# Kernel tuning notes

Measured on AMD Instinct MI355X. Metric: run time of the kernel, lower is better.

Reference implementation:

```python
import jax, jax.numpy as jnp
import numpy as np

EPS = 1e-6
DIAG_SIZE = 128  # triu band half-width (init kwarg diag_size)
NEG_INF = -1e9


def feature_map(x):
    # tanh feature map: phi(x) = tanh(x) + 1 (positive feature map)
    return jnp.tanh(x) + 1.0


def causal_dot_product(Q, K, V):
    # Q,K: [N,L,H,E], V: [N,L,H,D]
    # running KV state: S_l = sum_{s<=l} K_s V_s^T, materialized via cumsum
    kv = jnp.cumsum(jnp.einsum('nlhe,nlhd->nlhed', K, V), axis=1)  # [N,L,H,E,D]
    return jnp.einsum('nlhe,nlhed->nlhd', Q, kv)


def setup_inputs() -> dict:
    key = jax.random.key(0)
    k1, k2, k3 = jax.random.split(key, 3)
    N, L, H, E = 2, 2048, 8, 64
    queries = jax.random.normal(k1, (N, L, H, E), dtype=jnp.float32)
    keys = jax.random.normal(k2, (N, L, H, E), dtype=jnp.float32)
    values = jax.random.normal(k3, (N, L, H, E), dtype=jnp.float32)
    key_lengths_mask = jnp.ones((N, L), dtype=jnp.float32)  # all keys valid
    blend = jnp.full((1,), 0.9, dtype=jnp.float32)  # learned blend param (init 0.9)
    return {"queries": queries, "keys": keys, "values": values,
            "key_lengths_mask": key_lengths_mask, "blend": blend}


def reference(queries, keys, values, key_lengths_mask, blend):
    N, L, H, E = queries.shape
    # ---- linear attention path (kernel_1 = tanh, kernel_2 = 'none') ----
    Q1 = feature_map(queries)
    K1 = feature_map(keys) * key_lengths_mask[:, :, None, None]
    Z1 = 1.0 / (jnp.einsum('nlhi,nlhi->nlh', Q1, jnp.cumsum(K1, axis=1)) + EPS)
    LV = causal_dot_product(Q1, K1, values) * Z1[..., None]  # [N,L,H,D]
    # ---- full softmax attention path (banded by triu) ----
    softmax_temp = 1.0 / np.sqrt(E).astype(np.float32)
    QK = jnp.einsum('nlhe,nshe->nhls', queries, keys)  # [N,H,L,L]
    l_idx = jnp.arange(L)[:, None]
    s_idx = jnp.arange(L)[None, :]
    causal_add = jnp.where(s_idx <= l_idx, 0.0, NEG_INF)  # lower-triangular mask
    key_add = jnp.where(key_lengths_mask > 0, 0.0, NEG_INF)  # [N,L]
    logits = softmax_temp * (QK + causal_add[None, None] + key_add[:, None, None, :])
    A = jax.nn.softmax(logits, axis=-1)
    # torch.triu(A, diagonal=-diag_size): keep s >= l - diag_size
    band = s_idx >= (l_idx - DIAG_SIZE)
    A = jnp.where(band[None, None], A, 0.0)
    # dropout: eval mode (identity)
    SV = jnp.einsum('nhls,nshd->nlhd', A, values)
    b = blend[0]
    return b * SV + (1.0 - b) * LV
```

## Files before the change

### kernel.cpp

```cpp
#include <hip/hip_runtime.h>
#include <math.h>

#define N_ 2
#define L_ 2048
#define H_ 8
#define E_ 64
#define D_ 64
#define C_ 128
#define NC (L_/C_)
#define ROWSTRIDE (H_*E_)
#define TEMP 0.125f
#define EPS_F 1e-6f
#define NEG_INF_F (-1e9f)
#define CHUNK_WS (E_*D_ + E_)
#define NCHUNKS (N_*H_*NC)
#define TPAD 136
#define PPAD 72
#define PSTG 136

typedef __attribute__((ext_vector_type(8))) short short8;
typedef __attribute__((ext_vector_type(4))) float f32x4;

__device__ __forceinline__ short f2bf(float x) {
  unsigned u = __float_as_uint(x);
  u += 0x7fffu + ((u >> 16) & 1u);
  return (short)(u >> 16);
}
__device__ __forceinline__ float bf2f(short s) {
  return __uint_as_float(((unsigned)(unsigned short)s) << 16);
}
__device__ __forceinline__ float tanh1f(float x) {
  float e = __expf(-2.f * x);
  return 2.f * __builtin_amdgcn_rcpf(1.f + e);
}

template <typename F>
__device__ __forceinline__ void stage_tile(short* __restrict__ dst,
                                           const float* __restrict__ src, F f) {
  const int t = threadIdx.x;
#pragma unroll
  for (int it = 0; it < 4; ++it) {
    int gi = it * 256 + t;
    int row = gi >> 3, g = gi & 7;
    const float* p = src + row * ROWSTRIDE + g * 8;
    float4 a = *(const float4*)p;
    float4 b = *(const float4*)(p + 4);
    float xs[8] = {a.x, a.y, a.z, a.w, b.x, b.y, b.z, b.w};
    short8 v;
#pragma unroll
    for (int j = 0; j < 8; ++j) v[j] = f2bf(f(xs[j], row));
    *(short8*)(dst + row * 64 + (g ^ (row & 7)) * 8) = v;
  }
}

__device__ __forceinline__ short8 frag_ld(const short* __restrict__ buf,
                                          int rowbase, int hf, int lane) {
  int r = rowbase + (lane & 15);
  int g = (hf * 4 + (lane >> 4)) ^ (r & 7);
  return *(const short8*)(buf + r * 64 + g * 8);
}
__device__ __forceinline__ short8 frag_ldT(const short* __restrict__ buf,
                                           int nbase, int g, int lane) {
  int r = nbase + (lane & 15);
  return *(const short8*)(buf + r * TPAD + g * 8);
}
__device__ __forceinline__ short8 frag_ldP(const short* __restrict__ buf,
                                           int rowbase, int ks, int lane) {
  int r = rowbase + (lane & 15);
  int g = ks * 4 + (lane >> 4);
  return *(const short8*)(buf + r * PPAD + g * 8);
}

extern "C" __global__ void __launch_bounds__(256)
k_pre(const float* __restrict__ Q, const float* __restrict__ K,
      const float* __restrict__ V, const float* __restrict__ mask,
      float* __restrict__ ws, float* __restrict__ part,
      short* __restrict__ pd, short* __restrict__ pp) {
  __shared__ short lds[17408];
  __shared__ float fmsk[C_];
  short* ldsA = lds;
  short* ldsB = lds + 8704;
  const int orig = blockIdx.x;
  const int swz = (orig & 7) * 304 + (orig >> 3);
  const int t = threadIdx.x;
  const int w = t >> 6, lane = t & 63;
  const int col_lo = lane & 15;

  if (swz < 2176) {
    const int nh = swz / 136;
    const int p = swz - nh * 136;
    int qb = (int)((sqrtf(8.f * p + 1.f) - 1.f) * 0.5f);
    while ((qb + 1) * (qb + 2) / 2 <= p) ++qb;
    while (qb * (qb + 1) / 2 > p) --qb;
    const int kb = p - qb * (qb + 1) / 2;
    const int h = nh & (H_ - 1), n = nh >> 3;

    stage_tile(ldsA, Q + ((n * L_ + qb * C_) * H_ + h) * E_,
               [](float x, int) { return x; });
    stage_tile(ldsB, K + ((n * L_ + kb * C_) * H_ + h) * E_,
               [](float x, int) { return x; });
    if (t < C_) fmsk[t] = mask[n * L_ + kb * C_ + t];
    __syncthreads();

    const int rowbase = w * 32;
    short8 afr[2][2];
#pragma unroll
    for (int m = 0; m < 2; ++m)
#pragma unroll
      for (int hh = 0; hh < 2; ++hh)
        afr[m][hh] = frag_ld(ldsA, rowbase + 16 * m, hh, lane);

    f32x4 acc[2][8];
#pragma unroll
    for (int m = 0; m < 2; ++m)
#pragma unroll
      for (int c = 0; c < 8; ++c) acc[m][c] = (f32x4){0.f, 0.f, 0.f, 0.f};

#pragma unroll
    for (int c = 0; c < 8; ++c) {
      short8 b0 = frag_ld(ldsB, 16 * c, 0, lane);
      short8 b1 = frag_ld(ldsB, 16 * c, 1, lane);
#pragma unroll
      for (int m = 0; m < 2; ++m) {
        acc[m][c] = __builtin_amdgcn_mfma_f32_16x16x32_bf16(afr[m][0], b0, acc[m][c], 0, 0, 0);
        acc[m][c] = __builtin_amdgcn_mfma_f32_16x16x32_bf16(afr[m][1], b1, acc[m][c], 0, 0, 0);
      }
    }

    const bool diag = (kb == qb);
    const bool prev = (kb == qb - 1);
    const bool band = diag || prev;
    if (band) __syncthreads();

    float* pout = part + (size_t)(nh * NC + qb) * C_ * 16;
#pragma unroll
    for (int m = 0; m < 2; ++m) {
      const int rbase = rowbase + 16 * m + ((lane >> 4) << 2);
      float rs[4] = {0.f, 0.f, 0.f, 0.f};
#pragma unroll
      for (int c = 0; c < 8; ++c) {
        const int col = 16 * c + col_lo;
        const float madd = (fmsk[col] > 0.f) ? 0.f : NEG_INF_F;
#pragma unroll
        for (int reg = 0; reg < 4; ++reg) {
          float x = acc[m][c][reg] + madd;
          if (diag && col > rbase + reg) x += NEG_INF_F;
          float e = __expf(x * TEMP);
          rs[reg] += e;
          if (band) {
            if (prev && col < rbase + reg) e = 0.f;
            lds[(rbase + reg) * PSTG + col] = f2bf(e);
          }
        }
      }
#pragma unroll
      for (int off = 1; off < 16; off <<= 1) {
#pragma unroll
        for (int reg = 0; reg < 4; ++reg) rs[reg] += __shfl_xor(rs[reg], off);
      }
      if (col_lo == 0) {
#pragma unroll
        for (int reg = 0; reg < 4; ++reg) pout[(rbase + reg) * 16 + kb] = rs[reg];
      }
    }

    if (band) {
      __syncthreads();
      short* pt = (diag ? pd : pp) + (size_t)(nh * NC + qb) * (C_ * C_);
#pragma unroll
      for (int i = 0; i < 8; ++i) {
        int flat = i * 256 + t;
        int row = flat >> 4, g = flat & 15;
        *(short8*)(pt + row * C_ + g * 8) =
            *(const short8*)(lds + row * PSTG + g * 8);
      }
    }
  } else {
    const int id = swz - 2176;
    const int nh = id >> 4, c = id & 15;
    const int h = nh & (H_ - 1), n = nh >> 3;
    const int gbase = ((n * L_ + c * C_) * H_ + h) * E_;
    const int e = t & 63, sb = t >> 6;
    const int mbase = n * L_ + c * C_;
#pragma unroll
    for (int q = 0; q < 4; ++q) {
      int s0 = sb * 32 + q * 8;
      short8 kk, vv;
#pragma unroll
      for (int j = 0; j < 8; ++j) {
        float kx = K[gbase + (s0 + j) * ROWSTRIDE + e];
        kk[j] = f2bf(tanh1f(kx) * mask[mbase + s0 + j]);
        vv[j] = f2bf(V[gbase + (s0 + j) * ROWSTRIDE + e]);
      }
      *(short8*)(ldsA + e * TPAD + (s0 >> 3) * 8) = kk;
      *(short8*)(ldsB + e * TPAD + (s0 >> 3) * 8) = vv;
    }
    __syncthreads();

    f32x4 acc[4];
#pragma unroll
    for (int nn = 0; nn < 4; ++nn) acc[nn] = (f32x4){0.f, 0.f, 0.f, 0.f};
#pragma unroll
    for (int ks = 0; ks < 4; ++ks) {
      short8 a = frag_ldT(ldsB, 16 * w, ks * 4 + (lane >> 4), lane);
#pragma unroll
      for (int nn = 0; nn < 4; ++nn) {
        short8 b = frag_ldT(ldsA, 16 * nn, ks * 4 + (lane >> 4), lane);
        acc[nn] = __builtin_amdgcn_mfma_f32_16x16x32_bf16(a, b, acc[nn], 0, 0, 0);
      }
    }
    float* wsc = ws + (size_t)(nh * NC + c) * CHUNK_WS;
    const int drow = 16 * w + ((lane >> 4) << 2);
#pragma unroll
    for (int nn = 0; nn < 4; ++nn)
#pragma unroll
      for (int reg = 0; reg < 4; ++reg)
        wsc[(16 * nn + col_lo) * D_ + drow + reg] = acc[nn][reg];
    if (t < 64) {
      float s = 0.f;
#pragma unroll
      for (int g = 0; g < 16; ++g) {
        short8 v = *(const short8*)(ldsA + t * TPAD + g * 8);
#pragma unroll
        for (int j = 0; j < 8; ++j) s += bf2f(v[j]);
      }
      wsc[E_ * D_ + t] = s;
    }
  }
}

extern "C" __global__ void __launch_bounds__(256)
k_scan(float* __restrict__ ws) {
  const int bid = blockIdx.x;
  const int swz = (bid & 7) * 34 + (bid >> 3);
  const int nh = swz / 17, seg = swz - nh * 17;
  const int idx = seg * 256 + threadIdx.x;
  if (idx >= CHUNK_WS) return;
  float* base = ws + (size_t)nh * NC * CHUNK_WS + idx;
  float v[NC];
#pragma unroll
  for (int c = 0; c < NC; ++c) v[c] = base[(size_t)c * CHUNK_WS];
  float acc = 0.f;
#pragma unroll
  for (int c = 0; c < NC; ++c) {
    base[(size_t)c * CHUNK_WS] = acc;
    acc += v[c];
  }
}

extern "C" __global__ void __launch_bounds__(256, 2)
k_fused(const float* __restrict__ Q, const float* __restrict__ K,
        const float* __restrict__ V, const float* __restrict__ mask,
        const float* __restrict__ blend, const float* __restrict__ ws,
        const float* __restrict__ part, const short* __restrict__ pd,
        const short* __restrict__ pp, float* __restrict__ out) {
  __shared__ short kbuf[C_ * 64];
  __shared__ short kv[64 * TPAD];
  __shared__ short pbuf[64 * PPAD];
  __shared__ float zlds[64];
  __shared__ float dinv[64];
  __shared__ float ksum[E_];

  const int orig = blockIdx.x;
  const int swz = (orig & 7) * 64 + (orig >> 3);
  const int rh = swz & 1, qb = (swz >> 1) & (NC - 1), nh = swz >> 5;
  const int h = nh & (H_ - 1), n = nh >> 3;
  const int t = threadIdx.x;
  const int w = t >> 6, lane = t & 63;
  const int rowbase = w * 16;
  const int col_lo = lane & 15;
  const int rb = rowbase + ((lane >> 4) << 2);
  const int rtile0 = rh * 64 + rb;
  const int qgbase = ((n * L_ + qb * C_ + rh * 64) * H_ + h) * E_;
  const int kbase_chunk = ((n * L_ + qb * C_) * H_ + h) * E_;
  const float* wsc = ws + (size_t)(nh * NC + qb) * CHUNK_WS;
  const float bl = blend[0];
  const float ob = 1.f - bl;
  const int d = t & 63, sb = t >> 6;
  const bool haveprev = (qb > 0);
  const int kgp = ((n * L_ + (qb - 1) * C_) * H_ + h) * E_;

  {
    const float* mrow = mask + n * L_ + qb * C_;
#pragma unroll
    for (int it = 0; it < 4; ++it) {
      int gi = it * 256 + t, row = gi >> 3, g = gi & 7;
      const float* p = K + kbase_chunk + row * ROWSTRIDE + g * 8;
      float4 a = *(const float4*)p, b = *(const float4*)(p + 4);
      float km = mrow[row];
      float xs[8] = {a.x, a.y, a.z, a.w, b.x, b.y, b.z, b.w};
      short8 v1;
#pragma unroll
      for (int j = 0; j < 8; ++j) v1[j] = f2bf(tanh1f(xs[j]) * km);
      *(short8*)(kbuf + row * 64 + (g ^ (row & 7)) * 8) = v1;
    }
  }
  {
    int eb = t >> 6;
#pragma unroll
    for (int q = 0; q < 2; ++q) {
      int e0 = eb * 16 + q * 8;
      short8 v;
#pragma unroll
      for (int j = 0; j < 8; ++j) v[j] = f2bf(wsc[(e0 + j) * D_ + d]);
      *(short8*)(kv + d * TPAD + (e0 >> 3) * 8) = v;
    }
  }
  if (t < 64) {
    ksum[t] = wsc[E_ * D_ + t];
    const float* pb = part + ((size_t)(nh * NC + qb) * C_ + rh * 64 + t) * 16;
    float4 a = *(const float4*)pb, b = *(const float4*)(pb + 4);
    float4 c = *(const float4*)(pb + 8), d4 = *(const float4*)(pb + 12);
    float vv[16] = {a.x, a.y, a.z, a.w, b.x, b.y, b.z, b.w,
                    c.x, c.y, c.z, c.w, d4.x, d4.y, d4.z, d4.w};
    float s = 0.f;
#pragma unroll
    for (int j = 0; j < 16; ++j) s += (j <= qb) ? vv[j] : 0.f;
    dinv[t] = 1.f / s;
  }
  __syncthreads();

  short8 af1[2];
  {
    const float* qp = Q + qgbase + (rowbase + (lane & 15)) * ROWSTRIDE;
#pragma unroll
    for (int kh = 0; kh < 2; ++kh) {
      int c0 = (kh * 4 + (lane >> 4)) * 8;
      float4 a = *(const float4*)(qp + c0);
      float4 b = *(const float4*)(qp + c0 + 4);
      float xs[8] = {a.x, a.y, a.z, a.w, b.x, b.y, b.z, b.w};
#pragma unroll
      for (int j = 0; j < 8; ++j) af1[kh][j] = f2bf(tanh1f(xs[j]));
    }
  }
  f32x4 c1[8];
#pragma unroll
  for (int ct = 0; ct < 8; ++ct) c1[ct] = (f32x4){0.f, 0.f, 0.f, 0.f};
#pragma unroll
  for (int ct = 0; ct < 8; ++ct) {
    short8 b0 = frag_ld(kbuf, 16 * ct, 0, lane);
    short8 b1 = frag_ld(kbuf, 16 * ct, 1, lane);
    c1[ct] = __builtin_amdgcn_mfma_f32_16x16x32_bf16(af1[0], b0, c1[ct], 0, 0, 0);
    c1[ct] = __builtin_amdgcn_mfma_f32_16x16x32_bf16(af1[1], b1, c1[ct], 0, 0, 0);
  }
  {
    float zz = 0.f;
#pragma unroll
    for (int kh = 0; kh < 2; ++kh) {
      int cb = (kh * 4 + (lane >> 4)) * 8;
#pragma unroll
      for (int j = 0; j < 8; ++j) zz += bf2f(af1[kh][j]) * ksum[cb + j];
    }
    zz += __shfl_xor(zz, 16);
    zz += __shfl_xor(zz, 32);
    if (lane < 16) zlds[rowbase + lane] = zz;
  }
  float rs[4] = {0.f, 0.f, 0.f, 0.f};
#pragma unroll
  for (int ct = 0; ct < 8; ++ct) {
    int col = 16 * ct + col_lo;
#pragma unroll
    for (int reg = 0; reg < 4; ++reg) {
      if (col <= rtile0 + reg) rs[reg] += c1[ct][reg];
      else c1[ct][reg] = 0.f;
    }
  }
#pragma unroll
  for (int off = 1; off < 16; off <<= 1)
#pragma unroll
    for (int reg = 0; reg < 4; ++reg) rs[reg] += __shfl_xor(rs[reg], off);

  f32x4 accO[4];
#pragma unroll
  for (int nn = 0; nn < 4; ++nn) accO[nn] = (f32x4){0.f, 0.f, 0.f, 0.f};
#pragma unroll
  for (int ks = 0; ks < 2; ++ks) {
    short8 bf[4];
#pragma unroll
    for (int nn = 0; nn < 4; ++nn)
      bf[nn] = frag_ldT(kv, 16 * nn, ks * 4 + (lane >> 4), lane);
#pragma unroll
    for (int nn = 0; nn < 4; ++nn)
      accO[nn] = __builtin_amdgcn_mfma_f32_16x16x32_bf16(af1[ks], bf[nn], accO[nn], 0, 0, 0);
  }
  float zrf[4], sdv[4];
#pragma unroll
  for (int reg = 0; reg < 4; ++reg) {
    zrf[reg] = ob / (zlds[rb + reg] + rs[reg] + EPS_F);
    sdv[reg] = bl * dinv[rb + reg];
  }
#pragma unroll
  for (int nn = 0; nn < 4; ++nn)
#pragma unroll
    for (int reg = 0; reg < 4; ++reg) accO[nn][reg] *= zrf[reg];
#pragma unroll
  for (int ct = 0; ct < 8; ++ct)
#pragma unroll
    for (int reg = 0; reg < 4; ++reg) c1[ct][reg] *= zrf[reg];
  __syncthreads();

#pragma unroll
  for (int q = 0; q < 4; ++q) {
    int s0 = sb * 32 + q * 8;
    short8 v;
#pragma unroll
    for (int j = 0; j < 8; ++j) v[j] = f2bf(V[kbase_chunk + (s0 + j) * ROWSTRIDE + d]);
    *(short8*)(kv + d * TPAD + (s0 >> 3) * 8) = v;
  }
  __syncthreads();

#pragma unroll
  for (int hh = 0; hh < 2; ++hh) {
#pragma unroll
    for (int cc = 0; cc < 4; ++cc) {
      int ct = 4 * hh + cc, colh = 16 * cc + col_lo;
#pragma unroll
      for (int reg = 0; reg < 4; ++reg)
        pbuf[(rb + reg) * PPAD + colh] = f2bf(c1[ct][reg]);
    }
#pragma unroll
    for (int ks = 0; ks < 2; ++ks) {
      short8 ap = frag_ldP(pbuf, rowbase, ks, lane);
      short8 bv[4];
#pragma unroll
      for (int nn = 0; nn < 4; ++nn)
        bv[nn] = frag_ldT(kv, 16 * nn, 8 * hh + ks * 4 + (lane >> 4), lane);
#pragma unroll
      for (int nn = 0; nn < 4; ++nn)
        accO[nn] = __builtin_amdgcn_mfma_f32_16x16x32_bf16(ap, bv[nn], accO[nn], 0, 0, 0);
    }
  }

  f32x4 accS[4];
#pragma unroll
  for (int nn = 0; nn < 4; ++nn) accS[nn] = (f32x4){0.f, 0.f, 0.f, 0.f};
  {
    const short* ps = pd + (size_t)(nh * NC + qb) * (C_ * C_) + (size_t)(rh * 64) * C_;
#pragma unroll
    for (int hh = 0; hh < 2; ++hh) {
#pragma unroll
      for (int i = 0; i < 2; ++i) {
        int idx = i * 64 + lane;
        int rl = rowbase + (idx >> 3), g = idx & 7;
        short8 v = *(const short8*)(ps + (size_t)rl * C_ + 64 * hh + g * 8);
        *(short8*)(pbuf + rl * PPAD + g * 8) = v;
      }
#pragma unroll
      for (int ks = 0; ks < 2; ++ks) {
        short8 ap = frag_ldP(pbuf, rowbase, ks, lane);
        short8 bv[4];
#pragma unroll
        for (int nn = 0; nn < 4; ++nn)
          bv[nn] = frag_ldT(kv, 16 * nn, 8 * hh + ks * 4 + (lane >> 4), lane);
#pragma unroll
        for (int nn = 0; nn < 4; ++nn)
          accS[nn] = __builtin_amdgcn_mfma_f32_16x16x32_bf16(ap, bv[nn], accS[nn], 0, 0, 0);
      }
    }
  }

  if (haveprev) {
    __syncthreads();
#pragma unroll
    for (int q = 0; q < 4; ++q) {
      int s0 = sb * 32 + q * 8;
      short8 v;
#pragma unroll
      for (int j = 0; j < 8; ++j) v[j] = f2bf(V[kgp + (s0 + j) * ROWSTRIDE + d]);
      *(short8*)(kv + d * TPAD + (s0 >> 3) * 8) = v;
    }
    __syncthreads();

    const short* ps = pp + (size_t)(nh * NC + qb) * (C_ * C_) + (size_t)(rh * 64) * C_;
#pragma unroll
    for (int hh = 0; hh < 2; ++hh) {
#pragma unroll
      for (int i = 0; i < 2; ++i) {
        int idx = i * 64 + lane;
        int rl = rowbase + (idx >> 3), g = idx & 7;
        short8 v = *(const short8*)(ps + (size_t)rl * C_ + 64 * hh + g * 8);
        *(short8*)(pbuf + rl * PPAD + g * 8) = v;
      }
#pragma unroll
      for (int ks = 0; ks < 2; ++ks) {
        short8 ap = frag_ldP(pbuf, rowbase, ks, lane);
        short8 bv[4];
#pragma unroll
        for (int nn = 0; nn < 4; ++nn)
          bv[nn] = frag_ldT(kv, 16 * nn, 8 * hh + ks * 4 + (lane >> 4), lane);
#pragma unroll
        for (int nn = 0; nn < 4; ++nn)
          accS[nn] = __builtin_amdgcn_mfma_f32_16x16x32_bf16(ap, bv[nn], accS[nn], 0, 0, 0);
      }
    }
  }

#pragma unroll
  for (int nn = 0; nn < 4; ++nn)
#pragma unroll
    for (int reg = 0; reg < 4; ++reg)
      out[qgbase + (rb + reg) * ROWSTRIDE + 16 * nn + col_lo] =
          accO[nn][reg] + sdv[reg] * accS[nn][reg];
}

extern "C" void kernel_launch(void* const* d_in, const int* in_sizes, int n_in,
                              void* d_out, int out_size, void* d_ws, size_t ws_size,
                              hipStream_t stream) {
  (void)in_sizes; (void)n_in; (void)out_size; (void)ws_size;
  const float* Q = (const float*)d_in[0];
  const float* K = (const float*)d_in[1];
  const float* V = (const float*)d_in[2];
  const float* mask = (const float*)d_in[3];
  const float* blend = (const float*)d_in[4];
  float* out = (float*)d_out;
  float* ws = (float*)d_ws;
  float* part = ws + (size_t)NCHUNKS * CHUNK_WS;
  short* pd = (short*)(part + (size_t)NCHUNKS * C_ * 16);
  short* pp = pd + (size_t)NCHUNKS * C_ * C_;

  k_pre<<<dim3(2432), dim3(256), 0, stream>>>(Q, K, V, mask, ws, part, pd, pp);
  k_scan<<<dim3(272), dim3(256), 0, stream>>>(ws);
  k_fused<<<dim3(N_ * H_ * NC * 2), dim3(256), 0, stream>>>(Q, K, V, mask, blend, ws, part, pd, pp, out);
}
```

Baseline: 47.15 us.

## Split fused kernel output across two D-halves to double block count

The fused kernel now launches 1024 blocks instead of 512, each computing only 32 of the 64 output columns (a D-half), with the KV state and V tiles in LDS shrunk to 32 columns. This gives more parallelism across the GPU's CUs and lowers per-block register and LDS use. In exchange, the Q feature map, the QK^T block scores, the causal row sums and the K staging are now recomputed in both D-halves, and the launch-bounds occupancy hint is dropped.

```diff
diff --git a/kernel.cpp b/kernel.cpp
--- a/kernel.cpp
+++ b/kernel.cpp
@@ -248,22 +248,23 @@
   }
 }
 
-extern "C" __global__ void __launch_bounds__(256, 2)
+extern "C" __global__ void __launch_bounds__(256)
 k_fused(const float* __restrict__ Q, const float* __restrict__ K,
         const float* __restrict__ V, const float* __restrict__ mask,
         const float* __restrict__ blend, const float* __restrict__ ws,
         const float* __restrict__ part, const short* __restrict__ pd,
         const short* __restrict__ pp, float* __restrict__ out) {
   __shared__ short kbuf[C_ * 64];
-  __shared__ short kv[64 * TPAD];
+  __shared__ short kv[32 * TPAD];
   __shared__ short pbuf[64 * PPAD];
   __shared__ float zlds[64];
   __shared__ float dinv[64];
   __shared__ float ksum[E_];
 
   const int orig = blockIdx.x;
-  const int swz = (orig & 7) * 64 + (orig >> 3);
-  const int rh = swz & 1, qb = (swz >> 1) & (NC - 1), nh = swz >> 5;
+  const int swz = (orig & 7) * 128 + (orig >> 3);
+  const int dh = swz & 1, rh = (swz >> 1) & 1;
+  const int qb = (swz >> 2) & (NC - 1), nh = swz >> 6;
   const int h = nh & (H_ - 1), n = nh >> 3;
   const int t = threadIdx.x;
   const int w = t >> 6, lane = t & 63;
@@ -271,14 +272,15 @@
   const int col_lo = lane & 15;
   const int rb = rowbase + ((lane >> 4) << 2);
   const int rtile0 = rh * 64 + rb;
+  const int dd0 = dh * 32;
   const int qgbase = ((n * L_ + qb * C_ + rh * 64) * H_ + h) * E_;
   const int kbase_chunk = ((n * L_ + qb * C_) * H_ + h) * E_;
   const float* wsc = ws + (size_t)(nh * NC + qb) * CHUNK_WS;
   const float bl = blend[0];
   const float ob = 1.f - bl;
-  const int d = t & 63, sb = t >> 6;
   const bool haveprev = (qb > 0);
   const int kgp = ((n * L_ + (qb - 1) * C_) * H_ + h) * E_;
+  const int dloc = t & 31;
 
   {
     const float* mrow = mask + n * L_ + qb * C_;
@@ -296,15 +298,11 @@
     }
   }
   {
-    int eb = t >> 6;
-#pragma unroll
-    for (int q = 0; q < 2; ++q) {
-      int e0 = eb * 16 + q * 8;
-      short8 v;
-#pragma unroll
-      for (int j = 0; j < 8; ++j) v[j] = f2bf(wsc[(e0 + j) * D_ + d]);
-      *(short8*)(kv + d * TPAD + (e0 >> 3) * 8) = v;
-    }
+    int eb = t >> 5;
+    short8 v;
+#pragma unroll
+    for (int j = 0; j < 8; ++j) v[j] = f2bf(wsc[(eb * 8 + j) * D_ + dd0 + dloc]);
+    *(short8*)(kv + dloc * TPAD + eb * 8) = v;
   }
   if (t < 64) {
     ksum[t] = wsc[E_ * D_ + t];
@@ -370,17 +368,17 @@
 #pragma unroll
     for (int reg = 0; reg < 4; ++reg) rs[reg] += __shfl_xor(rs[reg], off);
 
-  f32x4 accO[4];
-#pragma unroll
-  for (int nn = 0; nn < 4; ++nn) accO[nn] = (f32x4){0.f, 0.f, 0.f, 0.f};
+  f32x4 accO[2];
+#pragma unroll
+  for (int nn = 0; nn < 2; ++nn) accO[nn] = (f32x4){0.f, 0.f, 0.f, 0.f};
 #pragma unroll
   for (int ks = 0; ks < 2; ++ks) {
-    short8 bf[4];
-#pragma unroll
-    for (int nn = 0; nn < 4; ++nn)
+    short8 bf[2];
+#pragma unroll
+    for (int nn = 0; nn < 2; ++nn)
       bf[nn] = frag_ldT(kv, 16 * nn, ks * 4 + (lane >> 4), lane);
 #pragma unroll
-    for (int nn = 0; nn < 4; ++nn)
+    for (int nn = 0; nn < 2; ++nn)
       accO[nn] = __builtin_amdgcn_mfma_f32_16x16x32_bf16(af1[ks], bf[nn], accO[nn], 0, 0, 0);
   }
   float zrf[4], sdv[4];
@@ -390,7 +388,7 @@
     sdv[reg] = bl * dinv[rb + reg];
   }
 #pragma unroll
-  for (int nn = 0; nn < 4; ++nn)
+  for (int nn = 0; nn < 2; ++nn)
 #pragma unroll
     for (int reg = 0; reg < 4; ++reg) accO[nn][reg] *= zrf[reg];
 #pragma unroll
@@ -399,13 +397,17 @@
     for (int reg = 0; reg < 4; ++reg) c1[ct][reg] *= zrf[reg];
   __syncthreads();
 
-#pragma unroll
-  for (int q = 0; q < 4; ++q) {
-    int s0 = sb * 32 + q * 8;
-    short8 v;
-#pragma unroll
-    for (int j = 0; j < 8; ++j) v[j] = f2bf(V[kbase_chunk + (s0 + j) * ROWSTRIDE + d]);
-    *(short8*)(kv + d * TPAD + (s0 >> 3) * 8) = v;
+  {
+    int sb8 = t >> 5;
+#pragma unroll
+    for (int q = 0; q < 2; ++q) {
+      int s0 = sb8 * 16 + q * 8;
+      short8 v;
+#pragma unroll
+      for (int j = 0; j < 8; ++j)
+        v[j] = f2bf(V[kbase_chunk + (s0 + j) * ROWSTRIDE + dd0 + dloc]);
+      *(short8*)(kv + dloc * TPAD + (s0 >> 3) * 8) = v;
+    }
   }
   __syncthreads();
 
@@ -421,19 +423,19 @@
 #pragma unroll
     for (int ks = 0; ks < 2; ++ks) {
       short8 ap = frag_ldP(pbuf, rowbase, ks, lane);
-      short8 bv[4];
-#pragma unroll
-      for (int nn = 0; nn < 4; ++nn)
+      short8 bv[2];
+#pragma unroll
+      for (int nn = 0; nn < 2; ++nn)
         bv[nn] = frag_ldT(kv, 16 * nn, 8 * hh + ks * 4 + (lane >> 4), lane);
 #pragma unroll
-      for (int nn = 0; nn < 4; ++nn)
+      for (int nn = 0; nn < 2; ++nn)
         accO[nn] = __builtin_amdgcn_mfma_f32_16x16x32_bf16(ap, bv[nn], accO[nn], 0, 0, 0);
     }
   }
 
-  f32x4 accS[4];
-#pragma unroll
-  for (int nn = 0; nn < 4; ++nn) accS[nn] = (f32x4){0.f, 0.f, 0.f, 0.f};
+  f32x4 accS[2];
+#pragma unroll
+  for (int nn = 0; nn < 2; ++nn) accS[nn] = (f32x4){0.f, 0.f, 0.f, 0.f};
   {
     const short* ps = pd + (size_t)(nh * NC + qb) * (C_ * C_) + (size_t)(rh * 64) * C_;
 #pragma unroll
@@ -448,12 +450,12 @@
 #pragma unroll
       for (int ks = 0; ks < 2; ++ks) {
         short8 ap = frag_ldP(pbuf, rowbase, ks, lane);
-        short8 bv[4];
-#pragma unroll
-        for (int nn = 0; nn < 4; ++nn)
+        short8 bv[2];
+#pragma unroll
+        for (int nn = 0; nn < 2; ++nn)
           bv[nn] = frag_ldT(kv, 16 * nn, 8 * hh + ks * 4 + (lane >> 4), lane);
 #pragma unroll
-        for (int nn = 0; nn < 4; ++nn)
+        for (int nn = 0; nn < 2; ++nn)
           accS[nn] = __builtin_amdgcn_mfma_f32_16x16x32_bf16(ap, bv[nn], accS[nn], 0, 0, 0);
       }
     }
@@ -461,13 +463,17 @@
 
   if (haveprev) {
     __syncthreads();
-#pragma unroll
-    for (int q = 0; q < 4; ++q) {
-      int s0 = sb * 32 + q * 8;
-      short8 v;
-#pragma unroll
-      for (int j = 0; j < 8; ++j) v[j] = f2bf(V[kgp + (s0 + j) * ROWSTRIDE + d]);
-      *(short8*)(kv + d * TPAD + (s0 >> 3) * 8) = v;
+    {
+      int sb8 = t >> 5;
+#pragma unroll
+      for (int q = 0; q < 2; ++q) {
+        int s0 = sb8 * 16 + q * 8;
+        short8 v;
+#pragma unroll
+        for (int j = 0; j < 8; ++j)
+          v[j] = f2bf(V[kgp + (s0 + j) * ROWSTRIDE + dd0 + dloc]);
+        *(short8*)(kv + dloc * TPAD + (s0 >> 3) * 8) = v;
+      }
     }
     __syncthreads();
 
@@ -484,22 +490,22 @@
 #pragma unroll
       for (int ks = 0; ks < 2; ++ks) {
         short8 ap = frag_ldP(pbuf, rowbase, ks, lane);
-        short8 bv[4];
-#pragma unroll
-        for (int nn = 0; nn < 4; ++nn)
+        short8 bv[2];
+#pragma unroll
+        for (int nn = 0; nn < 2; ++nn)
           bv[nn] = frag_ldT(kv, 16 * nn, 8 * hh + ks * 4 + (lane >> 4), lane);
 #pragma unroll
-        for (int nn = 0; nn < 4; ++nn)
+        for (int nn = 0; nn < 2; ++nn)
           accS[nn] = __builtin_amdgcn_mfma_f32_16x16x32_bf16(ap, bv[nn], accS[nn], 0, 0, 0);
       }
     }
   }
 
 #pragma unroll
-  for (int nn = 0; nn < 4; ++nn)
+  for (int nn = 0; nn < 2; ++nn)
 #pragma unroll
     for (int reg = 0; reg < 4; ++reg)
-      out[qgbase + (rb + reg) * ROWSTRIDE + 16 * nn + col_lo] =
+      out[qgbase + (rb + reg) * ROWSTRIDE + dd0 + 16 * nn + col_lo] =
           accO[nn][reg] + sdv[reg] * accS[nn][reg];
 }
 
@@ -520,5 +526,5 @@
 
   k_pre<<<dim3(2432), dim3(256), 0, stream>>>(Q, K, V, mask, ws, part, pd, pp);
   k_scan<<<dim3(272), dim3(256), 0, stream>>>(ws);
-  k_fused<<<dim3(N_ * H_ * NC * 2), dim3(256), 0, stream>>>(Q, K, V, mask, blend, ws, part, pd, pp, out);
-}
+  k_fused<<<dim3(1024), dim3(256), 0, stream>>>(Q, K, V, mask, blend, ws, part, pd, pp, out);
+}
```

Measured after the change: 51.89 us. +10.0%, slower.
